# Kernel tuning notes

Measured on AMD Instinct MI355X. Metric: run time of the kernel, lower is better.

Reference implementation:

```python
import jax, jax.numpy as jnp
import numpy as np


def _exp_levels(dx, depth):
    """Tensor-algebra exponential of a single increment dx [B, C]:
    level j is dx^{(x) j} / j!, flattened to [B, C^j]."""
    B = dx.shape[0]
    levels = [dx]
    for j in range(2, depth + 1):
        levels.append((jnp.einsum('bi,bj->bij', levels[-1], dx) / j).reshape(B, -1))
    return levels


def _chen_step(levels, dx, depth):
    """Chen's identity: sig(path * segment) = sig(path) (x) exp(dx).
    levels: tuple of [B, C^k] for k=1..depth. dx: [B, C]."""
    B = dx.shape[0]
    exps = _exp_levels(dx, depth)
    new = []
    for k in range(1, depth + 1):
        acc = levels[k - 1] + exps[k - 1]  # A_k * 1  +  1 * E_k
        for j in range(1, k):
            # A_{k-j} (x) E_j, flattened: [B, C^{k-j}] x [B, C^j] -> [B, C^k]
            acc = acc + jnp.einsum('bi,bj->bij', levels[k - j - 1], exps[j - 1]).reshape(B, -1)
        new.append(acc)
    return tuple(new)


def setup_inputs() -> dict:
    key = jax.random.key(0)
    path = jax.random.normal(key, (64, 512, 10), dtype=jnp.float32)
    return {"path": path, "depth": 4}


def reference(path, depth):
    # signature(path, depth, stream=False, basepoint=False, inverse=False,
    #           initial=None, scalar_term=False)
    dx = path[:, 1:] - path[:, :-1]  # [B, L-1, C] increments
    B = path.shape[0]
    # Initialise with the signature of the first segment: exp(dx_0).
    init = tuple(_exp_levels(dx[:, 0], depth))
    # Fold remaining segments via Chen's relation (a sequential scan; the
    # original's batch-trick is just a reassociation of this same product).
    dx_rest = jnp.swapaxes(dx[:, 1:], 0, 1)  # [L-2, B, C]

    def step(carry, d):
        return _chen_step(carry, d, depth), None

    carry, _ = jax.lax.scan(step, init, dx_rest)
    # Concatenate levels: output [B, C + C^2 + ... + C^depth]
    return jnp.concatenate(carry, axis=-1)
```

## Files before the change

kernel.cpp:

```cpp
#include <hip/hip_runtime.h>


#define CH      10
#define NSTEPS  511
#define ROW     12
#define SIGSZ   11110
#define NSEG    4
#define SEGLEN  128
#define WSSEG   11112

__global__ __launch_bounds__(256)
void sig_partial(const float* __restrict__ path, float* __restrict__ ws) {
    __shared__ __align__(16) float dxL[SEGLEN * ROW];

    const int tid  = threadIdx.x;
    const int b    = blockIdx.x >> 2;
    const int part = blockIdx.x & 3;
    const int seg  = blockIdx.y;
    const int s0   = seg * SEGLEN;

    const float* p = path + b * (512 * CH) + s0 * CH;
    for (int e = tid; e < SEGLEN * CH; e += 256) {
        int s = e / CH;
        int c = e - s * CH;
        dxL[s * ROW + c] = (s0 + s < NSTEPS) ? (p[e + CH] - p[e]) : 0.f;
    }
    __syncthreads();

    const int id = part * 256 + tid;
    if (id < 1000) {
        const int ci = id / 100;
        const int cj = (id / 10) % 10;
        const int ck = id % 10;

        float a1 = 0.f, a2 = 0.f, a3 = 0.f;
        float a4[10];
        #pragma unroll
        for (int l = 0; l < 10; ++l) a4[l] = 0.f;

        #pragma unroll 4
        for (int s = 0; s < SEGLEN; ++s) {
            const float* row = dxL + s * ROW;
            const float4 d0 = *(const float4*)(row);
            const float4 d1 = *(const float4*)(row + 4);
            const float2 d2 = *(const float2*)(row + 8);
            const float dxi = row[ci];
            const float dxj = row[cj];
            const float dxk = row[ck];

            const float p1 = a1 * (1.f / 6.f)  + dxi * (1.f / 24.f);
            const float q1 = a1 * 0.5f         + dxi * (1.f / 6.f);
            const float r1 = a1                + dxi * 0.5f;
            const float p2 = a2 * 0.5f + p1 * dxj;
            const float q2 = a2        + q1 * dxj;
            a2 += r1 * dxj;
            const float p3 = a3 + p2 * dxk;
            a3 += q2 * dxk;
            a1 += dxi;

            a4[0] += p3 * d0.x; a4[1] += p3 * d0.y;
            a4[2] += p3 * d0.z; a4[3] += p3 * d0.w;
            a4[4] += p3 * d1.x; a4[5] += p3 * d1.y;
            a4[6] += p3 * d1.z; a4[7] += p3 * d1.w;
            a4[8] += p3 * d2.x; a4[9] += p3 * d2.y;
        }

        float* ob = ws + (b * NSEG + seg) * WSSEG;
        float* o4 = ob + 1110 + id * 10;
        #pragma unroll
        for (int l = 0; l < 10; ++l) o4[l] = a4[l];
        ob[110 + id] = a3;
        if (ck == 0)            ob[10 + ci * 10 + cj] = a2;
        if (ck == 0 && cj == 0) ob[ci] = a1;
    }
}

__global__ __launch_bounds__(256)
void sig_combine(const float* __restrict__ ws, float* __restrict__ out) {
    const int tid  = threadIdx.x;
    const int b    = blockIdx.x >> 2;
    const int part = blockIdx.x & 3;
    const int id   = part * 256 + tid;
    if (id >= 1000) return;

    const int ci = id / 100;
    const int cj = (id / 10) % 10;
    const int ck = id % 10;

    const float* w0 = ws + b * NSEG * WSSEG;

    float a1 = w0[ci];
    float a2 = w0[10 + ci * 10 + cj];
    float a3 = w0[110 + id];
    float a4[10];
    #pragma unroll
    for (int l = 0; l < 10; ++l) a4[l] = w0[1110 + id * 10 + l];

    #pragma unroll
    for (int s = 1; s < NSEG; ++s) {
        const float* wb = w0 + s * WSSEG;
        const float b1i   = wb[ci];
        const float b1j   = wb[cj];
        const float b1k   = wb[ck];
        const float b2_ij = wb[10 + ci * 10 + cj];
        const float b2_jk = wb[10 + cj * 10 + ck];
        const float b3ijk = wb[110 + id];

        float b1v[10], b2k[10], b3jk[10], b4v[10];
        #pragma unroll
        for (int l = 0; l < 10; ++l) {
            b1v[l]  = wb[l];
            b2k[l]  = wb[10 + ck * 10 + l];
            b3jk[l] = wb[110 + (cj * 10 + ck) * 10 + l];
            b4v[l]  = wb[1110 + id * 10 + l];
        }

        #pragma unroll
        for (int l = 0; l < 10; ++l)
            a4[l] += a3 * b1v[l] + a2 * b2k[l] + a1 * b3jk[l] + b4v[l];
        a3 += a2 * b1k + a1 * b2_jk + b3ijk;
        a2 += a1 * b1j + b2_ij;
        a1 += b1i;
    }

    float* ob = out + b * SIGSZ;
    float* o4 = ob + 1110 + id * 10;
    #pragma unroll
    for (int l = 0; l < 10; ++l) o4[l] = a4[l];
    ob[110 + id] = a3;
    if (ck == 0)            ob[10 + ci * 10 + cj] = a2;
    if (ck == 0 && cj == 0) ob[ci] = a1;
}

extern "C" void kernel_launch(void* const* d_in, const int* in_sizes, int n_in,
                              void* d_out, int out_size, void* d_ws, size_t ws_size,
                              hipStream_t stream) {
    const float* path = (const float*)d_in[0];
    float* out = (float*)d_out;
    float* ws  = (float*)d_ws;

    sig_partial<<<dim3(256, NSEG), dim3(256), 0, stream>>>(path, ws);
    sig_combine<<<dim3(256), dim3(256), 0, stream>>>(ws, out);
}
```

Baseline: 89.82 us.

## Split path into more segments, precompute increments, stage combine operands in LDS

Adds a prep kernel that computes the path increments once, in both row-major padded and channel-transposed layouts. The partial kernel now uses 8 segments of 64 steps (2048 blocks) for more parallelism, reads per-thread i/j/k channels as float4 from a transposed LDS tile, and reads the full increment rows directly from global memory. The combine kernel stages each segment's low levels in shared memory. The cost is an extra launch, twice as many sequential combine steps, and global loads in the inner loop.

Result: slower. 116.1 us (+29.3%).

```diff
diff --git a/kernel.cpp b/kernel.cpp
--- a/kernel.cpp
+++ b/kernel.cpp
@@ -3,27 +3,67 @@
 
 #define CH      10
 #define NSTEPS  511
-#define ROW     12
 #define SIGSZ   11110
-#define NSEG    4
-#define SEGLEN  128
 #define WSSEG   11112
+#define NSEG    8
+#define SEGLEN  64
+#define PADT    68
+
+#define PART_OFF 0
+#define DXP_OFF  (64 * NSEG * WSSEG)
+#define DXT_OFF  (DXP_OFF + 64 * 512 * 12)
 
 __global__ __launch_bounds__(256)
-void sig_partial(const float* __restrict__ path, float* __restrict__ ws) {
-    __shared__ __align__(16) float dxL[SEGLEN * ROW];
+void sig_prep(const float* __restrict__ path, float* __restrict__ dxP,
+              float* __restrict__ dxT) {
+    const int b   = blockIdx.x;
+    const float* p = path + b * (512 * CH);
+    for (int e = threadIdx.x; e < 512 * CH; e += 256) {
+        const int s = e / CH;
+        const int c = e - s * CH;
+        const float v = (s < NSTEPS) ? (p[e + CH] - p[e]) : 0.f;
+        dxP[(size_t)b * (512 * 12) + s * 12 + c] = v;
+        dxT[(size_t)b * (CH * 512) + c * 512 + s] = v;
+    }
+}
+
+#define STEP(DXI, DXJ, DXK, DR) do {                                   \
+    const float4 d0 = *(const float4*)(DR);                            \
+    const float4 d1 = *(const float4*)((DR) + 4);                      \
+    const float2 d2 = *(const float2*)((DR) + 8);                      \
+    const float dxi = (DXI), dxj = (DXJ), dxk = (DXK);                 \
+    const float p1 = a1 * (1.f / 6.f) + dxi * (1.f / 24.f);            \
+    const float q1 = a1 * 0.5f        + dxi * (1.f / 6.f);             \
+    const float r1 = a1               + dxi * 0.5f;                    \
+    const float p2 = a2 * 0.5f + p1 * dxj;                             \
+    const float q2 = a2        + q1 * dxj;                             \
+    a2 += r1 * dxj;                                                    \
+    const float p3 = a3 + p2 * dxk;                                    \
+    a3 += q2 * dxk;                                                    \
+    a1 += dxi;                                                         \
+    a4[0] += p3 * d0.x; a4[1] += p3 * d0.y;                            \
+    a4[2] += p3 * d0.z; a4[3] += p3 * d0.w;                            \
+    a4[4] += p3 * d1.x; a4[5] += p3 * d1.y;                            \
+    a4[6] += p3 * d1.z; a4[7] += p3 * d1.w;                            \
+    a4[8] += p3 * d2.x; a4[9] += p3 * d2.y;                            \
+} while (0)
+
+__global__ __launch_bounds__(256)
+void sig_partial(const float* __restrict__ dxP, const float* __restrict__ dxT,
+                 float* __restrict__ ws) {
+    __shared__ __align__(16) float tl[CH * PADT];
 
     const int tid  = threadIdx.x;
-    const int b    = blockIdx.x >> 2;
-    const int part = blockIdx.x & 3;
-    const int seg  = blockIdx.y;
+    const int bx   = blockIdx.x;
+    const int b    = bx >> 5;
+    const int seg  = (bx >> 2) & 7;
+    const int part = bx & 3;
     const int s0   = seg * SEGLEN;
 
-    const float* p = path + b * (512 * CH) + s0 * CH;
-    for (int e = tid; e < SEGLEN * CH; e += 256) {
-        int s = e / CH;
-        int c = e - s * CH;
-        dxL[s * ROW + c] = (s0 + s < NSTEPS) ? (p[e + CH] - p[e]) : 0.f;
+    for (int e = tid; e < CH * SEGLEN; e += 256) {
+        const int c = e >> 6;
+        const int s = e & 63;
+        tl[c * PADT + s] = dxT[(size_t)(b * CH + c) * 512 + s0 + s];
     }
     __syncthreads();
 
@@ -38,34 +78,24 @@
         #pragma unroll
         for (int l = 0; l < 10; ++l) a4[l] = 0.f;
 
-        #pragma unroll 4
-        for (int s = 0; s < SEGLEN; ++s) {
-            const float* row = dxL + s * ROW;
-            const float4 d0 = *(const float4*)(row);
-            const float4 d1 = *(const float4*)(row + 4);
-            const float2 d2 = *(const float2*)(row + 8);
-            const float dxi = row[ci];
-            const float dxj = row[cj];
-            const float dxk = row[ck];
+        const float* ti = tl + ci * PADT;
+        const float* tj = tl + cj * PADT;
+        const float* tk = tl + ck * PADT;
+        const float* dp = dxP + (size_t)(b * 512 + s0) * 12;
 
-            const float p1 = a1 * (1.f / 6.f)  + dxi * (1.f / 24.f);
-            const float q1 = a1 * 0.5f         + dxi * (1.f / 6.f);
-            const float r1 = a1                + dxi * 0.5f;
-            const float p2 = a2 * 0.5f + p1 * dxj;
-            const float q2 = a2        + q1 * dxj;
-            a2 += r1 * dxj;
-            const float p3 = a3 + p2 * dxk;
-            a3 += q2 * dxk;
-            a1 += dxi;
-
-            a4[0] += p3 * d0.x; a4[1] += p3 * d0.y;
-            a4[2] += p3 * d0.z; a4[3] += p3 * d0.w;
-            a4[4] += p3 * d1.x; a4[5] += p3 * d1.y;
-            a4[6] += p3 * d1.z; a4[7] += p3 * d1.w;
-            a4[8] += p3 * d2.x; a4[9] += p3 * d2.y;
+        #pragma unroll 2
+        for (int s4 = 0; s4 < SEGLEN; s4 += 4) {
+            const float4 vi = *(const float4*)(ti + s4);
+            const float4 vj = *(const float4*)(tj + s4);
+            const float4 vk = *(const float4*)(tk + s4);
+            const float* dr = dp + s4 * 12;
+            STEP(vi.x, vj.x, vk.x, dr);
+            STEP(vi.y, vj.y, vk.y, dr + 12);
+            STEP(vi.z, vj.z, vk.z, dr + 24);
+            STEP(vi.w, vj.w, vk.w, dr + 36);
         }
 
-        float* ob = ws + (b * NSEG + seg) * WSSEG;
+        float* ob = ws + (size_t)(b * NSEG + seg) * WSSEG;
         float* o4 = ob + 1110 + id * 10;
         #pragma unroll
         for (int l = 0; l < 10; ++l) o4[l] = a4[l];
@@ -77,59 +107,69 @@
 
 __global__ __launch_bounds__(256)
 void sig_combine(const float* __restrict__ ws, float* __restrict__ out) {
+    __shared__ float B[1110];
+
     const int tid  = threadIdx.x;
     const int b    = blockIdx.x >> 2;
     const int part = blockIdx.x & 3;
     const int id   = part * 256 + tid;
-    if (id >= 1000) return;
+    const bool valid = (id < 1000);
 
     const int ci = id / 100;
     const int cj = (id / 10) % 10;
     const int ck = id % 10;
 
-    const float* w0 = ws + b * NSEG * WSSEG;
+    const float* w0 = ws + (size_t)b * NSEG * WSSEG;
 
-    float a1 = w0[ci];
-    float a2 = w0[10 + ci * 10 + cj];
-    float a3 = w0[110 + id];
+    float a1 = 0.f, a2 = 0.f, a3 = 0.f;
     float a4[10];
     #pragma unroll
-    for (int l = 0; l < 10; ++l) a4[l] = w0[1110 + id * 10 + l];
-
-    #pragma unroll
-    for (int s = 1; s < NSEG; ++s) {
-        const float* wb = w0 + s * WSSEG;
-        const float b1i   = wb[ci];
-        const float b1j   = wb[cj];
-        const float b1k   = wb[ck];
-        const float b2_ij = wb[10 + ci * 10 + cj];
-        const float b2_jk = wb[10 + cj * 10 + ck];
-        const float b3ijk = wb[110 + id];
-
-        float b1v[10], b2k[10], b3jk[10], b4v[10];
+    for (int l = 0; l < 10; ++l) a4[l] = 0.f;
+    if (valid) {
+        a1 = w0[ci];
+        a2 = w0[10 + ci * 10 + cj];
+        a3 = w0[110 + id];
         #pragma unroll
-        for (int l = 0; l < 10; ++l) {
-            b1v[l]  = wb[l];
-            b2k[l]  = wb[10 + ck * 10 + l];
-            b3jk[l] = wb[110 + (cj * 10 + ck) * 10 + l];
-            b4v[l]  = wb[1110 + id * 10 + l];
-        }
-
-        #pragma unroll
-        for (int l = 0; l < 10; ++l)
-            a4[l] += a3 * b1v[l] + a2 * b2k[l] + a1 * b3jk[l] + b4v[l];
-        a3 += a2 * b1k + a1 * b2_jk + b3ijk;
-        a2 += a1 * b1j + b2_ij;
-        a1 += b1i;
+        for (int l = 0; l < 10; ++l) a4[l] = w0[1110 + id * 10 + l];
     }
 
-    float* ob = out + b * SIGSZ;
-    float* o4 = ob + 1110 + id * 10;
-    #pragma unroll
-    for (int l = 0; l < 10; ++l) o4[l] = a4[l];
-    ob[110 + id] = a3;
-    if (ck == 0)            ob[10 + ci * 10 + cj] = a2;
-    if (ck == 0 && cj == 0) ob[ci] = a1;
+    for (int s = 1; s < NSEG; ++s) {
+        const float* wb = w0 + (size_t)s * WSSEG;
+        __syncthreads();
+        for (int e = tid; e < 1110; e += 256) B[e] = wb[e];
+        __syncthreads();
+
+        if (valid) {
+            const float b1i   = B[ci];
+            const float b1j   = B[cj];
+            const float b1k   = B[ck];
+            const float b2_ij = B[10 + ci * 10 + cj];
+            const float b2_jk = B[10 + cj * 10 + ck];
+            const float b3ijk = B[110 + id];
+
+            float b4v[10];
+            #pragma unroll
+            for (int l = 0; l < 10; ++l) b4v[l] = wb[1110 + id * 10 + l];
+
+            #pragma unroll
+            for (int l = 0; l < 10; ++l)
+                a4[l] += a3 * B[l] + a2 * B[10 + ck * 10 + l]
+                       + a1 * B[110 + (cj * 10 + ck) * 10 + l] + b4v[l];
+            a3 += a2 * b1k + a1 * b2_jk + b3ijk;
+            a2 += a1 * b1j + b2_ij;
+            a1 += b1i;
+        }
+    }
+
+    if (valid) {
+        float* ob = out + (size_t)b * SIGSZ;
+        float* o4 = ob + 1110 + id * 10;
+        #pragma unroll
+        for (int l = 0; l < 10; ++l) o4[l] = a4[l];
+        ob[110 + id] = a3;
+        if (ck == 0)            ob[10 + ci * 10 + cj] = a2;
+        if (ck == 0 && cj == 0) ob[ci] = a1;
+    }
 }
 
 extern "C" void kernel_launch(void* const* d_in, const int* in_sizes, int n_in,
@@ -139,6 +179,11 @@
     float* out = (float*)d_out;
     float* ws  = (float*)d_ws;
 
-    sig_partial<<<dim3(256, NSEG), dim3(256), 0, stream>>>(path, ws);
-    sig_combine<<<dim3(256), dim3(256), 0, stream>>>(ws, out);
+    float* part = ws + PART_OFF;
+    float* dxP  = ws + DXP_OFF;
+    float* dxT  = ws + DXT_OFF;
+
+    sig_prep   <<<dim3(64),   dim3(256), 0, stream>>>(path, dxP, dxT);
+    sig_partial<<<dim3(2048), dim3(256), 0, stream>>>(dxP, dxT, part);
+    sig_combine<<<dim3(256),  dim3(256), 0, stream>>>(part, out);
 }
```
